# Kernel optimization log

Measured on AMD Instinct MI355X. Metric: run time of the kernel, lower is better.

Reference implementation:

```python
import jax, jax.numpy as jnp
import numpy as np

DIM = 2048
H = 16
DK = 128
DV = 128
KCONV = 4
EPS = 1e-6
B = 2
S = 2048
KD = H * DK  # 2048
VD = H * DV  # 2048


def setup_inputs() -> dict:
    key = jax.random.key(0)
    ks = jax.random.split(key, 16)
    sc = 0.02
    inp = {
        "x": jax.random.normal(ks[0], (B, S, DIM), dtype=jnp.float32),
        "Wq": jax.random.normal(ks[1], (KD, DIM), dtype=jnp.float32) * sc,
        "Wk": jax.random.normal(ks[2], (KD, DIM), dtype=jnp.float32) * sc,
        "Wv": jax.random.normal(ks[3], (VD, DIM), dtype=jnp.float32) * sc,
        "Wa": jax.random.normal(ks[4], (H, DIM), dtype=jnp.float32) * sc,
        "Wb": jax.random.normal(ks[5], (H, DIM), dtype=jnp.float32) * sc,
        "Wg": jax.random.normal(ks[6], (VD, DIM), dtype=jnp.float32) * sc,
        "Wo": jax.random.normal(ks[7], (DIM, VD), dtype=jnp.float32) * sc,
        "cw_q": jax.random.normal(ks[8], (KD, KCONV), dtype=jnp.float32) * 0.3,
        "cb_q": jnp.zeros((KD,), dtype=jnp.float32),
        "cw_k": jax.random.normal(ks[9], (KD, KCONV), dtype=jnp.float32) * 0.3,
        "cb_k": jnp.zeros((KD,), dtype=jnp.float32),
        "cw_v": jax.random.normal(ks[10], (VD, KCONV), dtype=jnp.float32) * 0.3,
        "cb_v": jnp.zeros((VD,), dtype=jnp.float32),
        "A_log": jnp.zeros((H,), dtype=jnp.float32),
        "dt_bias": jnp.zeros((H,), dtype=jnp.float32),
        "norm_w": jnp.ones((VD,), dtype=jnp.float32),
    }
    return inp


def _causal_conv(x, w, b):
    # x: [B, S, C]; w: [C, K]; b: [C]. Depthwise causal conv (zero init state) + SiLU.
    Bb, Ss, C = x.shape
    xp = jnp.pad(x, ((0, 0), (KCONV - 1, 0), (0, 0)))
    out = b
    for j in range(KCONV):
        out = out + xp[:, j:j + Ss, :] * w[:, j]
    return jax.nn.silu(out)


def _l2norm(x):
    n = jnp.sqrt(jnp.sum(x * x, axis=-1, keepdims=True))
    return x / jnp.maximum(n, 1e-12)


def _forward(x, Wq, Wk, Wv, Wa, Wb, Wg, Wo, cw_q, cb_q, cw_k, cb_k, cw_v, cb_v,
             A_log, dt_bias, norm_w):
    Bb, Ss, _ = x.shape
    q = _causal_conv(x @ Wq.T, cw_q, cb_q)  # [B,S,KD]
    k = _causal_conv(x @ Wk.T, cw_k, cb_k)
    v = _causal_conv(x @ Wv.T, cw_v, cb_v)

    a = x @ Wa.T  # [B,S,H]
    b = x @ Wb.T
    g = jnp.exp(-jnp.exp(A_log)[None, None, :] * jax.nn.softplus(a + dt_bias[None, None, :]))
    beta = jax.nn.sigmoid(b)

    q = _l2norm(q.reshape(Bb, Ss, H, DK))
    k = _l2norm(k.reshape(Bb, Ss, H, DK))
    v = v.reshape(Bb, Ss, H, DV)

    S0 = jnp.zeros((Bb, H, DK, DV), dtype=x.dtype)

    def step(Sstate, inputs):
        q_t, k_t, v_t, g_t, beta_t = inputs  # [B,H,DK],[B,H,DK],[B,H,DV],[B,H],[B,H]
        retrieved = jnp.einsum('bhkv,bhk->bhv', Sstate, k_t)
        error = v_t - g_t[..., None] * retrieved
        update = k_t[..., :, None] * (beta_t[..., None] * error)[..., None, :]
        Snew = g_t[..., None, None] * Sstate + update
        o_t = jnp.einsum('bhkv,bhk->bhv', Snew, q_t)
        return Snew, o_t

    # scan over time: move time axis to front
    xs = (q.transpose(1, 0, 2, 3), k.transpose(1, 0, 2, 3), v.transpose(1, 0, 2, 3),
          g.transpose(1, 0, 2), beta.transpose(1, 0, 2))
    _, o = jax.lax.scan(step, S0, xs)  # o: [S,B,H,DV]
    o = o.transpose(1, 0, 2, 3).reshape(Bb, Ss, VD)

    # RMSNorm
    o = o * jax.lax.rsqrt(jnp.mean(o * o, axis=-1, keepdims=True) + EPS) * norm_w
    o = o * jax.nn.silu(x @ Wg.T)
    return o @ Wo.T


def reference(x, Wq, Wk, Wv, Wa, Wb, Wg, Wo, cw_q, cb_q, cw_k, cb_k, cw_v, cb_v,
              A_log, dt_bias, norm_w):
    return _forward(x, Wq, Wk, Wv, Wa, Wb, Wg, Wo, cw_q, cb_q, cw_k, cb_k,
                    cw_v, cb_v, A_log, dt_bias, norm_w)
```

## Files before the change

### kernel.cpp

```cpp
#include <hip/hip_runtime.h>

#define S_LEN   2048
#define NH      16
#define DIM     2048
#define KD      2048
#define VD      2048
#define MB      1048576ull
#define CT      64
#define NC      32

typedef short  short8  __attribute__((ext_vector_type(8)));
typedef short  short4v __attribute__((ext_vector_type(4)));
typedef float  floatx4 __attribute__((ext_vector_type(4)));

#define MFMA(a, b, c) __builtin_amdgcn_mfma_f32_16x16x32_bf16((a), (b), (c), 0, 0, 0)

__device__ inline short f2bf(float x) {
    unsigned u = __float_as_uint(x);
    unsigned r = (u + 0x7fffu + ((u >> 16) & 1u)) >> 16;
    return (short)r;
}
__device__ inline float bf2f(short s) {
    return __uint_as_float(((unsigned)(unsigned short)s) << 16);
}
__device__ inline float silu_f(float x) { return x / (1.f + __expf(-x)); }

__device__ inline short8 neg8(short8 a) {
    unsigned* p = (unsigned*)&a;
    p[0] ^= 0x80008000u; p[1] ^= 0x80008000u;
    p[2] ^= 0x80008000u; p[3] ^= 0x80008000u;
    return a;
}

__device__ inline void load_lds16(const void* g, void* l) {
    __builtin_amdgcn_global_load_lds(
        (const __attribute__((address_space(1))) unsigned int*)g,
        (__attribute__((address_space(3))) unsigned int*)l, 16, 0, 0);
}

__device__ inline void store_c(float* C, size_t idx, float v) { C[idx] = v; }
__device__ inline void store_c(short* C, size_t idx, float v) { C[idx] = f2bf(v); }

__device__ __forceinline__ void lds_barrier() {
    asm volatile("s_waitcnt lgkmcnt(0)" ::: "memory");
    __builtin_amdgcn_s_barrier();
}

#define VM(n_) asm volatile("s_waitcnt vmcnt(" #n_ ")" ::: "memory");

__global__ __launch_bounds__(256) void cvt_all_kernel(
    const float* __restrict__ x,  const float* __restrict__ Wq,
    const float* __restrict__ Wk, const float* __restrict__ Wv,
    const float* __restrict__ Wg, const float* __restrict__ Wo,
    short* __restrict__ xb,  short* __restrict__ Wqb, short* __restrict__ Wkb,
    short* __restrict__ Wvb, short* __restrict__ Wgb, short* __restrict__ Wob) {
    const float* in; short* out; int n8;
    switch (blockIdx.y) {
        case 0:  in = x;  out = xb;  n8 = 1048576; break;
        case 1:  in = Wq; out = Wqb; n8 = 524288;  break;
        case 2:  in = Wk; out = Wkb; n8 = 524288;  break;
        case 3:  in = Wv; out = Wvb; n8 = 524288;  break;
        case 4:  in = Wg; out = Wgb; n8 = 524288;  break;
        default: in = Wo; out = Wob; n8 = 524288;  break;
    }
    int i = blockIdx.x * 256 + threadIdx.x;
    if (i >= n8) return;
    float4 a = ((const float4*)in)[2 * i];
    float4 b = ((const float4*)in)[2 * i + 1];
    short8 o;
    o[0] = f2bf(a.x); o[1] = f2bf(a.y); o[2] = f2bf(a.z); o[3] = f2bf(a.w);
    o[4] = f2bf(b.x); o[5] = f2bf(b.y); o[6] = f2bf(b.z); o[7] = f2bf(b.w);
    ((short8*)out)[i] = o;
}


#define STAGE8(s_, isB_)                                                     \
    {                                                                        \
        const char* gsrc = (isB_) ? (const char*)Bw : (const char*)A;        \
        int t0 = (isB_) ? n0 : m0;                                           \
        char* dbase = smem + ((s_) & 3) * 32768 + (isB_) * 16384;            \
        _Pragma("unroll")                                                    \
        for (int ld = 0; ld < 2; ++ld) {                                     \
            int ch = ld * 8 + wave;                                          \
            int Pl = (ch << 10) + (lane << 4);                               \
            int Q  = Pl ^ (((lane >> 3) & 3) << 4);                          \
            const char* src = gsrc + ((size_t)(t0 + (Q >> 6)) << 12)         \
                              + ((size_t)(s_) << 6) + (Q & 63);              \
            load_lds16(src, dbase + (ch << 10));                             \
        }                                                                    \
    }

#define PHASE8(s_, qm_, LOADB_, STG, WAIT)                                   \
    {                                                                        \
        const char* sb = smem + ((s_) & 3) * 32768;                          \
        short8 af[4];                                                        \
        if (LOADB_) {                                                        \
            _Pragma("unroll")                                                \
            for (int nf = 0; nf < 4; ++nf)                                   \
                bfr[nf] = *(const short8*)(sb + 16384 +                      \
                    ((rowB_base + nf * 16) << 6) + qsw);                     \
        }                                                                    \
        _Pragma("unroll")                                                    \
        for (int mf = 0; mf < 4; ++mf)                                       \
            af[mf] = *(const short8*)(sb +                                   \
                ((rowA_base + (qm_) * 64 + mf * 16) << 6) + qsw);            \
        STG                                                                  \
        __builtin_amdgcn_s_barrier();                                        \
        asm volatile("s_waitcnt lgkmcnt(0)" ::: "memory");                   \
        __builtin_amdgcn_s_setprio(1);                                       \
        _Pragma("unroll")                                                    \
        for (int mf = 0; mf < 4; ++mf)                                       \
            _Pragma("unroll")                                                \
            for (int nf = 0; nf < 4; ++nf)                                   \
                acc[(qm_) * 4 + mf][nf] =                                    \
                    MFMA(af[mf], bfr[nf], acc[(qm_) * 4 + mf][nf]);          \
        __builtin_amdgcn_s_setprio(0);                                       \
        WAIT                                                                 \
        __builtin_amdgcn_s_barrier();                                        \
    }

template <typename OutT>
__device__ __forceinline__ void gemm8_tile(const short* __restrict__ A,
                                           const short* __restrict__ Bw,
                                           OutT* __restrict__ C, char* smem) {
    int x  = blockIdx.x;
    int xs = (x & 7) * 16 + (x >> 3);
    int m0 = (xs >> 3) * 256;
    int n0 = (xs & 7) * 256;
    int tid  = threadIdx.x;
    int wave = tid >> 6, lane = tid & 63;
    int l16  = lane & 15, quad = lane >> 4;
    int wm = wave >> 2, wn = wave & 3;
    int qsw = ((quad ^ ((l16 >> 1) & 3)) << 4);
    int rowA_base = wm * 128 + l16;
    int rowB_base = wn * 64 + l16;

    floatx4 acc[8][4];
#pragma unroll
    for (int i = 0; i < 8; ++i)
#pragma unroll
        for (int j = 0; j < 4; ++j) acc[i][j] = (floatx4){0.f, 0.f, 0.f, 0.f};
    short8 bfr[4];

    STAGE8(0, 0) STAGE8(0, 1)
    STAGE8(1, 0) STAGE8(1, 1)
    STAGE8(2, 0) STAGE8(2, 1)
    VM(8)
    __builtin_amdgcn_s_barrier();

#pragma unroll 1
    for (int T = 0; T < 30; ++T) {
        int s0 = 2 * T, s1 = 2 * T + 1, sa = 2 * T + 3, sb2 = 2 * T + 4;
        PHASE8(s0, 0, 1, STAGE8(sa, 0), )
        PHASE8(s0, 1, 0, STAGE8(sa, 1), VM(8))
        PHASE8(s1, 0, 1, STAGE8(sb2, 0), )
        PHASE8(s1, 1, 0, STAGE8(sb2, 1), VM(8))
    }
    PHASE8(60, 0, 1, STAGE8(63, 0), )
    PHASE8(60, 1, 0, STAGE8(63, 1), VM(8))
    PHASE8(61, 0, 1, , )
    PHASE8(61, 1, 0, , VM(4))
    PHASE8(62, 0, 1, , )
    PHASE8(62, 1, 0, , VM(0))
    PHASE8(63, 0, 1, , )
    PHASE8(63, 1, 0, , )

#pragma unroll
    for (int i = 0; i < 8; ++i) {
        int row0 = m0 + wm * 128 + (i >> 2) * 64 + (i & 3) * 16 + quad * 4;
#pragma unroll
        for (int nf = 0; nf < 4; ++nf) {
            int col = n0 + wn * 64 + nf * 16 + l16;
#pragma unroll
            for (int r = 0; r < 4; ++r)
                store_c(C, (size_t)(row0 + r) * 2048 + col, acc[i][nf][r]);
        }
    }
}

__global__ __launch_bounds__(512) void gemm8_qkvg(const short* __restrict__ A,
    const short* __restrict__ B0, const short* __restrict__ B1,
    const short* __restrict__ B2, const short* __restrict__ B3,
    short* __restrict__ C0, short* __restrict__ C1,
    short* __restrict__ C2, short* __restrict__ C3) {
    extern __shared__ char smem[];
    const short* Bw; short* C;
    switch (blockIdx.z) {
        case 0:  Bw = B0; C = C0; break;
        case 1:  Bw = B1; C = C1; break;
        case 2:  Bw = B2; C = C2; break;
        default: Bw = B3; C = C3; break;
    }
    gemm8_tile<short>(A, Bw, C, smem);
}

__global__ __launch_bounds__(512) void gemm8_out(const short* __restrict__ A,
    const short* __restrict__ Bw, float* __restrict__ C) {
    extern __shared__ char smem[];
    gemm8_tile<float>(A, Bw, C, smem);
}

__global__ __launch_bounds__(256) void ab_kernel(const float* __restrict__ x,
    const float* __restrict__ Wa, const float* __restrict__ Wb,
    const float* __restrict__ Alog, const float* __restrict__ dtb,
    float* __restrict__ gdec, float* __restrict__ beta) {
    __shared__ float xs[2048];
    __shared__ float red[32][9];
    int m = blockIdx.x, t = threadIdx.x;
    const float* xr = x + (size_t)m * DIM;
    for (int i = t; i < 512; i += 256) ((float4*)xs)[i] = ((const float4*)xr)[i];
    __syncthreads();
    int col = t >> 3, part = t & 7;
    const float* wr = (col < 16) ? (Wa + (size_t)col * DIM) : (Wb + (size_t)(col - 16) * DIM);
    float s = 0.f;
    int kb = part * 256;
#pragma unroll 4
    for (int k = 0; k < 256; k += 4) {
        float4 xv = *(const float4*)(xs + kb + k);
        float4 wv = *(const float4*)(wr + kb + k);
        s += xv.x * wv.x + xv.y * wv.y + xv.z * wv.z + xv.w * wv.w;
    }
    red[col][part] = s;
    __syncthreads();
    if (t < 32) {
        float a = 0.f;
#pragma unroll
        for (int p = 0; p < 8; ++p) a += red[t][p];
        if (t < 16) {
            float sp = a + dtb[t];
            float softp = (sp > 20.f) ? sp : log1pf(expf(sp));
            gdec[(size_t)m * NH + t] = expf(-expf(Alog[t]) * softp);
        } else {
            int h = t - 16;
            beta[(size_t)m * NH + h] = 1.f / (1.f + expf(-a));
        }
    }
}

__global__ __launch_bounds__(256) void conv_kernel(
    const short* __restrict__ qr, const short* __restrict__ kr, const short* __restrict__ vr,
    const float* __restrict__ cwq, const float* __restrict__ cbq,
    const float* __restrict__ cwk, const float* __restrict__ cbk,
    const float* __restrict__ cwv, const float* __restrict__ cbv,
    short* __restrict__ qn, short* __restrict__ kn, short* __restrict__ vc) {
    int gw   = blockIdx.x * 4 + (threadIdx.x >> 6);
    int lane = threadIdx.x & 63;
    int h  = gw & (NH - 1);
    int m  = gw >> 4;
    int tt = m & (S_LEN - 1);
    int c  = h * 128 + lane * 2;
    size_t rowbase = (size_t)m * KD + c;

    float4 wq0 = ((const float4*)cwq)[c], wq1 = ((const float4*)cwq)[c + 1];
    float4 wk0 = ((const float4*)cwk)[c], wk1 = ((const float4*)cwk)[c + 1];
    float4 wv0 = ((const float4*)cwv)[c], wv1 = ((const float4*)cwv)[c + 1];
    float q0 = cbq[c], q1 = cbq[c + 1];
    float k0 = cbk[c], k1 = cbk[c + 1];
    float v0 = cbv[c], v1 = cbv[c + 1];
    const float* wq0a = (const float*)&wq0; const float* wq1a = (const float*)&wq1;
    const float* wk0a = (const float*)&wk0; const float* wk1a = (const float*)&wk1;
    const float* wv0a = (const float*)&wv0; const float* wv1a = (const float*)&wv1;
#pragma unroll
    for (int j = 0; j < 4; ++j) {
        int ts = tt - 3 + j;
        if (ts >= 0) {
            long long rb = (long long)rowbase + (long long)(j - 3) * KD;
            unsigned uq = *(const unsigned*)(qr + rb);
            unsigned uk = *(const unsigned*)(kr + rb);
            unsigned uv = *(const unsigned*)(vr + rb);
            q0 += bf2f((short)(uq & 0xffff)) * wq0a[j]; q1 += bf2f((short)(uq >> 16)) * wq1a[j];
            k0 += bf2f((short)(uk & 0xffff)) * wk0a[j]; k1 += bf2f((short)(uk >> 16)) * wk1a[j];
            v0 += bf2f((short)(uv & 0xffff)) * wv0a[j]; v1 += bf2f((short)(uv >> 16)) * wv1a[j];
        }
    }
    q0 = silu_f(q0); q1 = silu_f(q1);
    k0 = silu_f(k0); k1 = silu_f(k1);
    v0 = silu_f(v0); v1 = silu_f(v1);

    float sq = q0 * q0 + q1 * q1;
    float sk = k0 * k0 + k1 * k1;
#pragma unroll
    for (int off = 1; off < 64; off <<= 1) {
        sq += __shfl_xor(sq, off);
        sk += __shfl_xor(sk, off);
    }
    float iq = 1.f / fmaxf(sqrtf(sq), 1e-12f);
    float ik = 1.f / fmaxf(sqrtf(sk), 1e-12f);
    unsigned oq = (unsigned)(unsigned short)f2bf(q0 * iq) | ((unsigned)(unsigned short)f2bf(q1 * iq) << 16);
    unsigned ok = (unsigned)(unsigned short)f2bf(k0 * ik) | ((unsigned)(unsigned short)f2bf(k1 * ik) << 16);
    unsigned ov = (unsigned)(unsigned short)f2bf(v0)      | ((unsigned)(unsigned short)f2bf(v1)      << 16);
    *(unsigned*)(qn + rowbase) = oq;
    *(unsigned*)(kn + rowbase) = ok;
    *(unsigned*)(vc + rowbase) = ov;
}

__global__ __launch_bounds__(256) void solve_kernel(
    const short* __restrict__ kn, const short* __restrict__ vn,
    const float* __restrict__ gdec, const float* __restrict__ beta,
    short* __restrict__ UvT, short* __restrict__ Tk) {
    __shared__ short Pn[64][72];
    __shared__ short Pt[64][72];
    __shared__ short UT[128][72];
    __shared__ float Ls[64];
    __shared__ float Bs[64];

    int wg   = blockIdx.x;
    int half = wg & 1;
    int c    = (wg >> 1) & 31;
    int bh   = wg >> 6;
    int b = bh >> 4, h = bh & 15;
    int tid = threadIdx.x;
    int wave = tid >> 6, lane = tid & 63;
    int quad = lane >> 4, l16 = lane & 15;

    const short* Kb = kn + ((size_t)(b * S_LEN + c * CT)) * KD + h * 128;
    const short* Vb = vn + ((size_t)(b * S_LEN + c * CT)) * KD + h * 128;

    if (wave == 0) {
        float lg = __logf(gdec[((size_t)(b * S_LEN + c * CT) + lane) * NH + h]);
#pragma unroll
        for (int off = 1; off < 64; off <<= 1) {
            float y = __shfl_up(lg, off);
            if (lane >= off) lg += y;
        }
        Ls[lane] = lg;
        Bs[lane] = beta[((size_t)(b * S_LEN + c * CT) + lane) * NH + h];
    }
    __syncthreads();

    {
        floatx4 acc[4];
#pragma unroll
        for (int i = 0; i < 4; ++i) acc[i] = (floatx4){0.f, 0.f, 0.f, 0.f};
        for (int ks = 0; ks < 4; ++ks) {
            short8 af = *(const short8*)(Kb + (size_t)(wave * 16 + l16) * KD + ks * 32 + quad * 8);
#pragma unroll
            for (int it = 0; it < 4; ++it) {
                short8 bf = *(const short8*)(Kb + (size_t)(it * 16 + l16) * KD + ks * 32 + quad * 8);
                acc[it] = MFMA(af, bf, acc[it]);
            }
        }
#pragma unroll
        for (int it = 0; it < 4; ++it) {
            int icol = it * 16 + l16;
#pragma unroll
            for (int r = 0; r < 4; ++r) {
                int trow = wave * 16 + quad * 4 + r;
                float v = 0.f;
                if (icol < trow) v = -Bs[trow] * __expf(Ls[trow] - Ls[icol]) * acc[it][r];
                short bv = f2bf(v);
                Pn[trow][icol] = bv;
                Pt[icol][trow] = bv;
            }
        }
    }

    {
        const short* src = half ? Kb : Vb;
        int tr = tid >> 2, seg = (tid & 3) * 32;
        float s = Bs[tr] * (half ? __expf(Ls[tr]) : 1.f);
#pragma unroll
        for (int j = 0; j < 4; ++j) {
            short8 d = *(const short8*)(src + (size_t)tr * KD + seg + j * 8);
#pragma unroll
            for (int e = 0; e < 8; ++e)
                UT[seg + j * 8 + e][tr] = f2bf(bf2f(d[e]) * s);
        }
    }
    __syncthreads();

    for (int iter = 0; iter < 6; ++iter) {
        floatx4 acc[8];
#pragma unroll
        for (int nt = 0; nt < 8; ++nt) {
            short4v u4 = *(const short4v*)&UT[nt * 16 + l16][wave * 16 + quad * 4];
            floatx4 a;
#pragma unroll
            for (int e = 0; e < 4; ++e) a[e] = bf2f(u4[e]);
            acc[nt] = a;
        }
        for (int ks = 0; ks < 2; ++ks) {
            short8 af = *(const short8*)&Pn[wave * 16 + l16][ks * 32 + quad * 8];
#pragma unroll
            for (int nt = 0; nt < 8; ++nt) {
                short8 bf = *(const short8*)&UT[nt * 16 + l16][ks * 32 + quad * 8];
                acc[nt] = MFMA(af, bf, acc[nt]);
            }
        }
        __syncthreads();
        if (iter < 5) {
#pragma unroll
            for (int nt = 0; nt < 8; ++nt) {
                short4v w4;
#pragma unroll
                for (int e = 0; e < 4; ++e) w4[e] = f2bf(acc[nt][e]);
                *(short4v*)&UT[nt * 16 + l16][wave * 16 + quad * 4] = w4;
            }
            floatx4 pacc[4];
#pragma unroll
            for (int it = 0; it < 4; ++it) pacc[it] = (floatx4){0.f, 0.f, 0.f, 0.f};
            for (int ks = 0; ks < 2; ++ks) {
                short8 paf = *(const short8*)&Pn[wave * 16 + l16][ks * 32 + quad * 8];
#pragma unroll
                for (int it = 0; it < 4; ++it) {
                    short8 pbf = *(const short8*)&Pt[it * 16 + l16][ks * 32 + quad * 8];
                    pacc[it] = MFMA(paf, pbf, pacc[it]);
                }
            }
            __syncthreads();
#pragma unroll
            for (int it = 0; it < 4; ++it) {
                int icol = it * 16 + l16;
#pragma unroll
                for (int r = 0; r < 4; ++r) {
                    int trow = wave * 16 + quad * 4 + r;
                    short bv = f2bf(pacc[it][r]);
                    Pn[trow][icol] = bv;
                    Pt[icol][trow] = bv;
                }
            }
            __syncthreads();
        } else {
            size_t cb = (size_t)(bh * NC + c);
            if (half == 0) {
                int usw = (((wave * 2 + (quad >> 1)) ^ (l16 & 7)) << 3) + ((quad & 1) << 2);
#pragma unroll
                for (int nt = 0; nt < 8; ++nt) {
                    short4v w4;
#pragma unroll
                    for (int e = 0; e < 4; ++e) w4[e] = f2bf(acc[nt][e]);
                    *(short4v*)(UvT + (cb * 128 + nt * 16 + l16) * 64 + usw) = w4;
                }
            } else {
#pragma unroll
                for (int nt = 0; nt < 8; ++nt)
#pragma unroll
                    for (int r = 0; r < 4; ++r) {
                        int trow = wave * 16 + quad * 4 + r;
                        int colsw = (((nt * 2 + (l16 >> 3)) ^ (trow & 7)) << 3) + (l16 & 7);
                        Tk[(cb * 64 + trow) * 128 + colsw] = f2bf(acc[nt][r]);
                    }
            }
        }
    }
}

__global__ __launch_bounds__(256) void prepb_kernel(
    const short* __restrict__ qn, const short* __restrict__ kn,
    const float* __restrict__ gdec,
    short* __restrict__ Wb_, short* __restrict__ Qg,
    short* __restrict__ KtT, float* __restrict__ gam63) {
    __shared__ short KT[128][72];
    __shared__ float Ls[64];
    int wg = blockIdx.x;
    int c = wg & 31, bh = wg >> 5;
    int b = bh >> 4, h = bh & 15;
    int tid = threadIdx.x, wave = tid >> 6, lane = tid & 63;
    int quad = lane >> 4, l16 = lane & 15;
    const short* Qb = qn + ((size_t)(b * S_LEN + c * CT)) * KD + h * 128;
    const short* Kb = kn + ((size_t)(b * S_LEN + c * CT)) * KD + h * 128;

    if (wave == 0) {
        float lg = __logf(gdec[((size_t)(b * S_LEN + c * CT) + lane) * NH + h]);
#pragma unroll
        for (int off = 1; off < 64; off <<= 1) {
            float y = __shfl_up(lg, off);
            if (lane >= off) lg += y;
        }
        Ls[lane] = lg;
    }
    __syncthreads();
    size_t cb = (size_t)(bh * NC + c);
    if (tid == 0) gam63[cb] = __expf(Ls[63]);

    {
        floatx4 acc[4];
#pragma unroll
        for (int i = 0; i < 4; ++i) acc[i] = (floatx4){0.f, 0.f, 0.f, 0.f};
        for (int ks = 0; ks < 4; ++ks) {
            short8 af = *(const short8*)(Qb + (size_t)(wave * 16 + l16) * KD + ks * 32 + quad * 8);
#pragma unroll
            for (int it = 0; it < 4; ++it) {
                short8 bf = *(const short8*)(Kb + (size_t)(it * 16 + l16) * KD + ks * 32 + quad * 8);
                acc[it] = MFMA(af, bf, acc[it]);
            }
        }
#pragma unroll
        for (int it = 0; it < 4; ++it) {
            int icol = it * 16 + l16;
#pragma unroll
            for (int r = 0; r < 4; ++r) {
                int trow = wave * 16 + quad * 4 + r;
                float v = (icol <= trow) ? __expf(Ls[trow] - Ls[icol]) * acc[it][r] : 0.f;
                int colsw = (((it * 2 + (l16 >> 3)) ^ (trow & 7)) << 3) + (l16 & 7);
                Wb_[(cb * 64 + trow) * 64 + colsw] = f2bf(v);
            }
        }
    }

    {
        int tr = tid >> 2, seg = (tid & 3) * 32;
        float sq = __expf(Ls[tr]);
        float sk = __expf(Ls[63] - Ls[tr]);
#pragma unroll
        for (int j = 0; j < 4; ++j) {
            short8 dq = *(const short8*)(Qb + (size_t)tr * KD + seg + j * 8);
            short8 dk = *(const short8*)(Kb + (size_t)tr * KD + seg + j * 8);
            short8 oq;
#pragma unroll
            for (int e = 0; e < 8; ++e) {
                oq[e] = f2bf(bf2f(dq[e]) * sq);
                KT[seg + j * 8 + e][tr] = f2bf(bf2f(dk[e]) * sk);
            }
            int ch = (tid & 3) * 4 + j;
            *(short8*)(Qg + (cb * 64 + tr) * 128 + ((ch ^ (tr & 7)) << 3)) = oq;
        }
    }
    __syncthreads();
    {
        int dk = tid >> 1, seg = (tid & 1) * 32;
#pragma unroll
        for (int j = 0; j < 4; ++j) {
            short8 v = *(const short8*)&KT[dk][seg + j * 8];
            int ch = (tid & 1) * 4 + j;
            *(short8*)(KtT + (cb * 128 + dk) * 64 + ((ch ^ (dk & 7)) << 3)) = v;
        }
    }
}

__global__ __launch_bounds__(256, 1) void seq_kernel(
    const short* __restrict__ UvT, const short* __restrict__ Tk,
    const short* __restrict__ Wb_, const short* __restrict__ Qg,
    const short* __restrict__ KtT, const float* __restrict__ gam63,
    short* __restrict__ ob) {
    extern __shared__ char smem[];
    const int BUF = 65536;
    const int TKO = 0, QGO = 16384, KTO = 32768, UVO = 49152, WO = 57344;
    short (*ST)[136] = (short (*)[136])(smem + 131072);
    short (*UTs)[72] = (short (*)[72])(smem + 131072 + 17408);

    int wg = blockIdx.x;
    int vh = wg & 1, bh = wg >> 1;
    int b = bh >> 4, h = bh & 15;
    int tid = threadIdx.x, wave = tid >> 6, lane = tid & 63;
    int quad = lane >> 4, l16 = lane & 15;
    int swk = l16 & 7;

    for (int i = tid; i < 64 * 136; i += 256) ((short*)(smem + 131072))[i] = 0;
    floatx4 sacc[8];
#pragma unroll
    for (int i = 0; i < 8; ++i) sacc[i] = (floatx4){0.f, 0.f, 0.f, 0.f};

    size_t cb0 = (size_t)bh * NC;
    int row16 = wave * 16 + l16;
    int chq[4];
#pragma unroll
    for (int ks = 0; ks < 4; ++ks) chq[ks] = (((ks * 4 + quad) ^ swk) << 4);
    int uvoff = (((wave * 2 + (quad >> 1)) ^ swk) << 4) + ((quad & 1) << 3);

#define STAGE_CHUNK(bsel_, c_)                                                       \
    {                                                                                \
        char* dst = smem + (bsel_) * BUF;                                            \
        size_t cbs = cb0 + (c_);                                                     \
        const char* gt = (const char*)Tk  + cbs * 16384 + wave * 1024 + lane * 16;   \
        const char* gq = (const char*)Qg  + cbs * 16384 + wave * 1024 + lane * 16;   \
        const char* gk = (const char*)KtT + cbs * 16384 + wave * 1024 + lane * 16;   \
        const char* gu = (const char*)UvT + cbs * 16384 + (size_t)vh * 8192 + wave * 1024 + lane * 16; \
        const char* gw = (const char*)Wb_ + cbs * 8192  + wave * 1024 + lane * 16;   \
        _Pragma("unroll")                                                            \
        for (int it = 0; it < 4; ++it) {                                             \
            load_lds16(gt + it * 4096, dst + TKO + it * 4096 + wave * 1024);         \
            load_lds16(gq + it * 4096, dst + QGO + it * 4096 + wave * 1024);         \
            load_lds16(gk + it * 4096, dst + KTO + it * 4096 + wave * 1024);         \
        }                                                                            \
        _Pragma("unroll")                                                            \
        for (int it = 0; it < 2; ++it) {                                             \
            load_lds16(gu + it * 4096, dst + UVO + it * 4096 + wave * 1024);         \
            load_lds16(gw + it * 4096, dst + WO  + it * 4096 + wave * 1024);         \
        }                                                                            \
    }

    STAGE_CHUNK(0, 0)
    float gamA = gam63[cb0];
    __syncthreads();

#pragma unroll 1
    for (int c = 0; c < NC; ++c) {
        float gamN = 0.f;
        if (c + 1 < NC) {
            gamN = gam63[cb0 + c + 1];
            STAGE_CHUNK((c + 1) & 1, c + 1)
        }
        const char* bufc = smem + (c & 1) * BUF;

        floatx4 uacc[4], oacc[4];
#pragma unroll
        for (int vt = 0; vt < 4; ++vt) {
            short4v u4 = *(const short4v*)(bufc + UVO + (vt * 16 + l16) * 128 + uvoff);
            floatx4 a;
#pragma unroll
            for (int e = 0; e < 4; ++e) a[e] = bf2f(u4[e]);
            uacc[vt] = a;
            oacc[vt] = (floatx4){0.f, 0.f, 0.f, 0.f};
        }
#pragma unroll
        for (int ks = 0; ks < 4; ++ks) {
            short8 tkf = *(const short8*)(bufc + TKO + row16 * 256 + chq[ks]);
            short8 qgf = *(const short8*)(bufc + QGO + row16 * 256 + chq[ks]);
            short8 afT = neg8(tkf);
#pragma unroll
            for (int vt = 0; vt < 4; ++vt) {
                short8 bf = *(const short8*)&ST[vt * 16 + l16][ks * 32 + quad * 8];
                uacc[vt] = MFMA(afT, bf, uacc[vt]);
                oacc[vt] = MFMA(qgf, bf, oacc[vt]);
            }
        }
#pragma unroll
        for (int vt = 0; vt < 4; ++vt) {
            short4v w4;
#pragma unroll
            for (int e = 0; e < 4; ++e) w4[e] = f2bf(uacc[vt][e]);
            *(short4v*)&UTs[vt * 16 + l16][wave * 16 + quad * 4] = w4;
        }
        lds_barrier();
#pragma unroll
        for (int ks = 0; ks < 2; ++ks) {
            short8 wf = *(const short8*)(bufc + WO + row16 * 128 + chq[ks]);
#pragma unroll
            for (int vt = 0; vt < 4; ++vt) {
                short8 bf = *(const short8*)&UTs[vt * 16 + l16][ks * 32 + quad * 8];
                oacc[vt] = MFMA(wf, bf, oacc[vt]);
            }
        }
#pragma unroll
        for (int vt = 0; vt < 4; ++vt)
#pragma unroll
            for (int r = 0; r < 4; ++r) {
                int m = b * S_LEN + c * CT + wave * 16 + quad * 4 + r;
                ob[(size_t)m * VD + h * 128 + vh * 64 + vt * 16 + l16] = f2bf(oacc[vt][r]);
            }
#pragma unroll
        for (int dt = 0; dt < 8; ++dt)
#pragma unroll
            for (int e = 0; e < 4; ++e) sacc[dt][e] *= gamA;
#pragma unroll
        for (int ks = 0; ks < 2; ++ks) {
            short8 af = *(const short8*)&UTs[wave * 16 + l16][ks * 32 + quad * 8];
#pragma unroll
            for (int dt = 0; dt < 8; ++dt) {
                short8 ktf = *(const short8*)(bufc + KTO + (dt * 16 + l16) * 128 + chq[ks]);
                sacc[dt] = MFMA(af, ktf, sacc[dt]);
            }
        }
#pragma unroll
        for (int dt = 0; dt < 8; ++dt)
#pragma unroll
            for (int r = 0; r < 4; ++r)
                ST[wave * 16 + quad * 4 + r][dt * 16 + l16] = f2bf(sacc[dt][r]);

        if (c + 1 < NC) {
            asm volatile("s_waitcnt lgkmcnt(0)" ::: "memory");
            VM(16)
            __builtin_amdgcn_s_barrier();
        }
        gamA = gamN;
    }
#undef STAGE_CHUNK
}

__global__ __launch_bounds__(256) void rms_gate_kernel(
    const short* __restrict__ o, const short* __restrict__ graw,
    const float* __restrict__ nw, short* __restrict__ og) {
    __shared__ float red[4];
    int m = blockIdx.x, t = threadIdx.x;
    short8 a = ((const short8*)(o + (size_t)m * VD))[t];
    float av[8];
#pragma unroll
    for (int i = 0; i < 8; ++i) av[i] = bf2f(a[i]);
    float ss = 0.f;
#pragma unroll
    for (int i = 0; i < 8; ++i) ss += av[i] * av[i];
#pragma unroll
    for (int off = 1; off < 64; off <<= 1) ss += __shfl_xor(ss, off);
    if ((t & 63) == 0) red[t >> 6] = ss;
    __syncthreads();
    float tot = red[0] + red[1] + red[2] + red[3];
    float sc = rsqrtf(tot * (1.f / VD) + 1e-6f);
    short8 gv = ((const short8*)(graw + (size_t)m * VD))[t];
    float4 n0 = ((const float4*)nw)[2 * t];
    float4 n1 = ((const float4*)nw)[2 * t + 1];
    const float* na = (const float*)&n0;
    const float* nb = (const float*)&n1;
    short8 ov;
#pragma unroll
    for (int i = 0; i < 4; ++i) ov[i]     = f2bf(av[i]     * sc * na[i] * silu_f(bf2f(gv[i])));
#pragma unroll
    for (int i = 0; i < 4; ++i) ov[i + 4] = f2bf(av[i + 4] * sc * nb[i] * silu_f(bf2f(gv[i + 4])));
    ((short8*)(og + (size_t)m * VD))[t] = ov;
}

extern "C" void kernel_launch(void* const* d_in, const int* in_sizes, int n_in,
                              void* d_out, int out_size, void* d_ws, size_t ws_size,
                              hipStream_t stream) {
    const float* x    = (const float*)d_in[0];
    const float* Wq   = (const float*)d_in[1];
    const float* Wk   = (const float*)d_in[2];
    const float* Wv   = (const float*)d_in[3];
    const float* Wa   = (const float*)d_in[4];
    const float* Wb   = (const float*)d_in[5];
    const float* Wg   = (const float*)d_in[6];
    const float* Wo   = (const float*)d_in[7];
    const float* cwq  = (const float*)d_in[8];
    const float* cbq  = (const float*)d_in[9];
    const float* cwk  = (const float*)d_in[10];
    const float* cbk  = (const float*)d_in[11];
    const float* cwv  = (const float*)d_in[12];
    const float* cbv  = (const float*)d_in[13];
    const float* Alog = (const float*)d_in[14];
    const float* dtb  = (const float*)d_in[15];
    const float* nw   = (const float*)d_in[16];

    char* ws = (char*)d_ws;
    short* Wob = (short*)(ws);
    short* xb  = (short*)(ws + 8 * MB);
    short* Wqb = (short*)(ws + 24 * MB);
    short* Wkb = (short*)(ws + 32 * MB);
    short* Wvb = (short*)(ws + 40 * MB);
    short* Wgb = (short*)(ws + 48 * MB);
    short* qrb = (short*)(ws + 56 * MB);
    short* krb = (short*)(ws + 72 * MB);
    short* vrb = (short*)(ws + 88 * MB);
    short* grb = (short*)(ws + 104 * MB);
    short* qnb = (short*)(ws + 8 * MB);
    short* knb = (short*)(ws + 24 * MB);
    short* vnb = (short*)(ws + 40 * MB);
    float* gdec = (float*)(ws + 120 * MB);
    float* beta = (float*)(ws + 120 * MB + 262144);
    short* ob  = qrb;
    short* ogb = krb;
    short* UvT  = (short*)(ws + 121 * MB);
    short* Tkb  = (short*)(ws + 137 * MB);
    short* Wbuf = (short*)(ws + 153 * MB);
    short* Qgb  = (short*)(ws + 161 * MB);
    short* KtT  = (short*)(ws + 177 * MB);
    float* gm63 = (float*)(ws + 193 * MB);

    static bool attr_done = false;
    if (!attr_done) {
        hipFuncSetAttribute((const void*)gemm8_qkvg,
                            hipFuncAttributeMaxDynamicSharedMemorySize, 131072);
        hipFuncSetAttribute((const void*)gemm8_out,
                            hipFuncAttributeMaxDynamicSharedMemorySize, 131072);
        hipFuncSetAttribute((const void*)seq_kernel,
                            hipFuncAttributeMaxDynamicSharedMemorySize, 157696);
        attr_done = true;
    }

    cvt_all_kernel<<<dim3(4096, 6), 256, 0, stream>>>(x, Wq, Wk, Wv, Wg, Wo,
                                                      xb, Wqb, Wkb, Wvb, Wgb, Wob);

    ab_kernel<<<4096, 256, 0, stream>>>(x, Wa, Wb, Alog, dtb, gdec, beta);

    gemm8_qkvg<<<dim3(128, 1, 4), 512, 131072, stream>>>(xb, Wqb, Wkb, Wvb, Wgb,
                                                         qrb, krb, vrb, grb);

    conv_kernel<<<16384, 256, 0, stream>>>(qrb, krb, vrb,
                                           cwq, cbq, cwk, cbk, cwv, cbv, qnb, knb, vnb);

    solve_kernel<<<2048, 256, 0, stream>>>(knb, vnb, gdec, beta, UvT, Tkb);
    prepb_kernel<<<1024, 256, 0, stream>>>(qnb, knb, gdec, Wbuf, Qgb, KtT, gm63);
    seq_kernel<<<64, 256, 157696, stream>>>(UvT, Tkb, Wbuf, Qgb, KtT, gm63, ob);

    rms_gate_kernel<<<4096, 256, 0, stream>>>(ob, grb, nw, ogb);

    gemm8_out<<<dim3(128, 1, 1), 512, 131072, stream>>>(ogb, Wob, (float*)d_out);
}
```

Before: 723.3 us.

## Software-pipeline LDS fragment reads with MFMA and halve barriers in GEMM tile

Restructures the GEMM main loop so the LDS fragment reads for the next half-tile are issued before the MFMA block of the current half-tile, using double-buffered A and B register fragments. This leaves one barrier per k-stage instead of two per half-phase, and lets LDS latency overlap matrix math. It also adds a minimum-occupancy hint of 2 to the launch bounds, which caps per-thread registers. That cap risks spilling, since the extra fragment registers raise register pressure.

```diff
diff --git a/kernel.cpp b/kernel.cpp
--- a/kernel.cpp
+++ b/kernel.cpp
@@ -44,6 +44,12 @@
 __device__ __forceinline__ void lds_barrier() {
     asm volatile("s_waitcnt lgkmcnt(0)" ::: "memory");
     __builtin_amdgcn_s_barrier();
+}
+
+__device__ __forceinline__ void boundary_barrier() {
+    asm volatile("s_waitcnt lgkmcnt(0)" ::: "memory");
+    __builtin_amdgcn_s_barrier();
+    asm volatile("" ::: "memory");
 }
 
 #define VM(n_) asm volatile("s_waitcnt vmcnt(" #n_ ")" ::: "memory");
@@ -90,33 +96,34 @@
         }                                                                    \
     }
 
-#define PHASE8(s_, qm_, LOADB_, STG, WAIT)                                   \
+#define RD_AF(dst_, s_, qm_)                                                 \
     {                                                                        \
-        const char* sb = smem + ((s_) & 3) * 32768;                          \
-        short8 af[4];                                                        \
-        if (LOADB_) {                                                        \
-            _Pragma("unroll")                                                \
-            for (int nf = 0; nf < 4; ++nf)                                   \
-                bfr[nf] = *(const short8*)(sb + 16384 +                      \
-                    ((rowB_base + nf * 16) << 6) + qsw);                     \
-        }                                                                    \
+        const char* sb_ = smem + ((s_) & 3) * 32768;                         \
         _Pragma("unroll")                                                    \
         for (int mf = 0; mf < 4; ++mf)                                       \
-            af[mf] = *(const short8*)(sb +                                   \
+            dst_[mf] = *(const short8*)(sb_ +                                \
                 ((rowA_base + (qm_) * 64 + mf * 16) << 6) + qsw);            \
-        STG                                                                  \
-        __builtin_amdgcn_s_barrier();                                        \
-        asm volatile("s_waitcnt lgkmcnt(0)" ::: "memory");                   \
+    }
+
+#define RD_BF(dst_, s_)                                                      \
+    {                                                                        \
+        const char* sb_ = smem + ((s_) & 3) * 32768 + 16384;                 \
+        _Pragma("unroll")                                                    \
+        for (int nf = 0; nf < 4; ++nf)                                       \
+            dst_[nf] = *(const short8*)(sb_ +                                \
+                ((rowB_base + nf * 16) << 6) + qsw);                         \
+    }
+
+#define MM(qm_, af_, bf_)                                                    \
+    {                                                                        \
         __builtin_amdgcn_s_setprio(1);                                       \
         _Pragma("unroll")                                                    \
         for (int mf = 0; mf < 4; ++mf)                                       \
             _Pragma("unroll")                                                \
             for (int nf = 0; nf < 4; ++nf)                                   \
                 acc[(qm_) * 4 + mf][nf] =                                    \
-                    MFMA(af[mf], bfr[nf], acc[(qm_) * 4 + mf][nf]);          \
+                    MFMA(af_[mf], bf_[nf], acc[(qm_) * 4 + mf][nf]);         \
         __builtin_amdgcn_s_setprio(0);                                       \
-        WAIT                                                                 \
-        __builtin_amdgcn_s_barrier();                                        \
     }
 
 template <typename OutT>
@@ -140,30 +147,58 @@
     for (int i = 0; i < 8; ++i)
 #pragma unroll
         for (int j = 0; j < 4; ++j) acc[i][j] = (floatx4){0.f, 0.f, 0.f, 0.f};
-    short8 bfr[4];
+    short8 af0[4], af1[4], bfA[4], bfB[4];
 
     STAGE8(0, 0) STAGE8(0, 1)
     STAGE8(1, 0) STAGE8(1, 1)
     STAGE8(2, 0) STAGE8(2, 1)
     VM(8)
-    __builtin_amdgcn_s_barrier();
+    boundary_barrier();
+    RD_AF(af0, 0, 0) RD_BF(bfA, 0)
 
 #pragma unroll 1
-    for (int T = 0; T < 30; ++T) {
-        int s0 = 2 * T, s1 = 2 * T + 1, sa = 2 * T + 3, sb2 = 2 * T + 4;
-        PHASE8(s0, 0, 1, STAGE8(sa, 0), )
-        PHASE8(s0, 1, 0, STAGE8(sa, 1), VM(8))
-        PHASE8(s1, 0, 1, STAGE8(sb2, 0), )
-        PHASE8(s1, 1, 0, STAGE8(sb2, 1), VM(8))
-    }
-    PHASE8(60, 0, 1, STAGE8(63, 0), )
-    PHASE8(60, 1, 0, STAGE8(63, 1), VM(8))
-    PHASE8(61, 0, 1, , )
-    PHASE8(61, 1, 0, , VM(4))
-    PHASE8(62, 0, 1, , )
-    PHASE8(62, 1, 0, , VM(0))
-    PHASE8(63, 0, 1, , )
-    PHASE8(63, 1, 0, , )
+    for (int sp = 0; sp < 60; sp += 2) {
+        STAGE8(sp + 3, 0)
+        RD_AF(af1, sp, 1)
+        MM(0, af0, bfA)
+        STAGE8(sp + 3, 1)
+        VM(8)
+        boundary_barrier();
+        RD_AF(af0, sp + 1, 0) RD_BF(bfB, sp + 1)
+        MM(1, af1, bfA)
+        STAGE8(sp + 4, 0)
+        RD_AF(af1, sp + 1, 1)
+        MM(0, af0, bfB)
+        STAGE8(sp + 4, 1)
+        VM(8)
+        boundary_barrier();
+        RD_AF(af0, sp + 2, 0) RD_BF(bfA, sp + 2)
+        MM(1, af1, bfB)
+    }
+
+    STAGE8(63, 0)
+    RD_AF(af1, 60, 1)
+    MM(0, af0, bfA)
+    STAGE8(63, 1)
+    VM(8)
+    boundary_barrier();
+    RD_AF(af0, 61, 0) RD_BF(bfB, 61)
+    MM(1, af1, bfA)
+    RD_AF(af1, 61, 1)
+    MM(0, af0, bfB)
+    VM(4)
+    boundary_barrier();
+    RD_AF(af0, 62, 0) RD_BF(bfA, 62)
+    MM(1, af1, bfB)
+    RD_AF(af1, 62, 1)
+    MM(0, af0, bfA)
+    VM(0)
+    boundary_barrier();
+    RD_AF(af0, 63, 0) RD_BF(bfB, 63)
+    MM(1, af1, bfA)
+    RD_AF(af1, 63, 1)
+    MM(0, af0, bfB)
+    MM(1, af1, bfB)
 
 #pragma unroll
     for (int i = 0; i < 8; ++i) {
@@ -178,7 +213,7 @@
     }
 }
 
-__global__ __launch_bounds__(512) void gemm8_qkvg(const short* __restrict__ A,
+__global__ __launch_bounds__(512, 2) void gemm8_qkvg(const short* __restrict__ A,
     const short* __restrict__ B0, const short* __restrict__ B1,
     const short* __restrict__ B2, const short* __restrict__ B3,
     short* __restrict__ C0, short* __restrict__ C1,
@@ -194,7 +229,7 @@
     gemm8_tile<short>(A, Bw, C, smem);
 }
 
-__global__ __launch_bounds__(512) void gemm8_out(const short* __restrict__ A,
+__global__ __launch_bounds__(512, 2) void gemm8_out(const short* __restrict__ A,
     const short* __restrict__ Bw, float* __restrict__ C) {
     extern __shared__ char smem[];
     gemm8_tile<float>(A, Bw, C, smem);
```

Measured after the change: 703.0 us. 2.8% less time.
